# Optimization experiments

Measured on AMD Instinct MI355X. Metric: run time of the kernel, lower is better.

## Reference

```python
import jax, jax.numpy as jnp
import numpy as np

EPS = 1e-5
LOCAL_WINDOW = 256
NUM_HEADS = 16


def _layernorm(x, g, b):
    m = jnp.mean(x, axis=-1, keepdims=True)
    v = jnp.mean(jnp.square(x - m), axis=-1, keepdims=True)
    return (x - m) * jax.lax.rsqrt(v + EPS) * g + b


def _rotate_half(x):
    x1, x2 = jnp.split(x, 2, axis=-1)
    return jnp.concatenate([-x2, x1], axis=-1)


def _rope_cos_sin(s, d, base=10000.0):
    half = d // 2
    inv_freq = 1.0 / base ** (jnp.arange(half, dtype=jnp.float32) / float(half))
    t = jnp.arange(s, dtype=jnp.float32)
    freqs = jnp.einsum('s,d->sd', t, inv_freq)          # [s, half]
    emb = jnp.concatenate([freqs, freqs], axis=-1)       # [s, d]
    return jnp.cos(emb)[None, None, :, :], jnp.sin(emb)[None, None, :, :]


def setup_inputs() -> dict:
    key = jax.random.key(0)
    ks = jax.random.split(key, 8)
    B, S, D, F = 2, 2048, 1024, 4096
    sc = lambda d: 1.0 / np.sqrt(d)
    return {
        'x': jax.random.normal(ks[0], (B, S, D), jnp.float32),
        'w_qkv': jax.random.normal(ks[1], (D, 3 * D), jnp.float32) * sc(D),
        'w_out': jax.random.normal(ks[2], (D, D), jnp.float32) * sc(D),
        'g1': jnp.ones((D,), jnp.float32),
        'b1': jnp.zeros((D,), jnp.float32),
        'g2': jnp.ones((D,), jnp.float32),
        'b2': jnp.zeros((D,), jnp.float32),
        'w_gate': jax.random.normal(ks[3], (D, F), jnp.float32) * sc(D),
        'b_gate': jnp.zeros((F,), jnp.float32),
        'w_up': jax.random.normal(ks[4], (D, F), jnp.float32) * sc(D),
        'b_up': jnp.zeros((F,), jnp.float32),
        'w_down': jax.random.normal(ks[5], (F, D), jnp.float32) * sc(F),
        'b_down': jnp.zeros((D,), jnp.float32),
    }


def reference(x, w_qkv, w_out, g1, b1, g2, b2, w_gate, b_gate, w_up, b_up, w_down, b_down):
    B, S, D = x.shape
    H = NUM_HEADS
    hd = D // H

    # ---- pre-norm + RoPE self-attention ----
    y = _layernorm(x, g1, b1)
    qkv = jnp.einsum('bsd,de->bse', y, w_qkv)
    q, k, v = jnp.split(qkv, 3, axis=-1)
    split_heads = lambda t: t.reshape(B, S, H, hd).transpose(0, 2, 1, 3)  # [b,h,s,hd]
    q, k, v = split_heads(q), split_heads(k), split_heads(v)

    cos, sin = _rope_cos_sin(S, hd)
    q = q * cos + _rotate_half(q) * sin
    k = k * cos + _rotate_half(k) * sin

    scale = float(hd) ** -0.5
    logits = jnp.einsum('bhid,bhjd->bhij', q, k) * scale

    i = jnp.arange(S)[:, None]
    j = jnp.arange(S)[None, :]
    can = (jnp.abs(j - i) <= LOCAL_WINDOW) & (j <= i)    # local + causal band
    logits = jnp.where(can[None, None], logits, jnp.float32(-1e9))

    attn = jax.nn.softmax(logits, axis=-1)
    o = jnp.einsum('bhij,bhjd->bhid', attn, v)
    o = o.transpose(0, 2, 1, 3).reshape(B, S, D)
    x = x + jnp.einsum('bsd,de->bse', o, w_out)

    # ---- pre-norm + SwiGLU MLP ----
    y = _layernorm(x, g2, b2)
    gate = jnp.einsum('bsd,df->bsf', y, w_gate) + b_gate
    up = jnp.einsum('bsd,df->bsf', y, w_up) + b_up
    gated = gate * jax.nn.silu(up)
    x = x + jnp.einsum('bsf,fd->bsd', gated, w_down) + b_down
    return x
```

## Files before the change

kernel.cpp:

```cpp
#include <hip/hip_runtime.h>

typedef unsigned short u16;
typedef unsigned long long u64;
typedef __attribute__((ext_vector_type(8))) short bf16x8;
typedef __attribute__((ext_vector_type(4))) float f32x4;

__device__ inline u16 f2bf(float f) {
  unsigned int u = __float_as_uint(f);
  u += 0x7fffu + ((u >> 16) & 1u);
  return (u16)(u >> 16);
}
__device__ inline float bf2f(u16 h) { return __uint_as_float(((unsigned int)h) << 16); }

__device__ inline void gload_lds16(const void* gp, void* lp) {
  __builtin_amdgcn_global_load_lds(
      (const __attribute__((address_space(1))) unsigned int*)gp,
      (__attribute__((address_space(3))) unsigned int*)lp, 16, 0, 0);
}

__global__ __launch_bounds__(256) void ln_kernel(const float* __restrict__ x,
                                                 const float* __restrict__ g,
                                                 const float* __restrict__ beta,
                                                 u16* __restrict__ y) {
  __shared__ float red[8];
  const int row = blockIdx.x;
  const int t = threadIdx.x;
  const float4 xv = *(const float4*)(x + (long)row * 1024 + t * 4);
  float s = xv.x + xv.y + xv.z + xv.w;
  float sq = xv.x * xv.x + xv.y * xv.y + xv.z * xv.z + xv.w * xv.w;
#pragma unroll
  for (int d = 1; d < 64; d <<= 1) {
    s += __shfl_xor(s, d);
    sq += __shfl_xor(sq, d);
  }
  if ((t & 63) == 0) { red[t >> 6] = s; red[4 + (t >> 6)] = sq; }
  __syncthreads();
  s = red[0] + red[1] + red[2] + red[3];
  sq = red[4] + red[5] + red[6] + red[7];
  const float mean = s * (1.f / 1024.f);
  const float var = sq * (1.f / 1024.f) - mean * mean;
  const float inv = rsqrtf(var + 1e-5f);
  float xe[4] = {xv.x, xv.y, xv.z, xv.w};
  u16 ov[4];
#pragma unroll
  for (int e = 0; e < 4; ++e)
    ov[e] = f2bf((xe[e] - mean) * inv * g[t * 4 + e] + beta[t * 4 + e]);
  *(u64*)(y + (long)row * 1024 + t * 4) = *(u64*)ov;
}

__global__ __launch_bounds__(256) void transpose_bf16(const float* __restrict__ in,
                                                      u16* __restrict__ out,
                                                      int R, int C) {
  __shared__ float tile[64][33];
  const int t = threadIdx.x;
  const int tx = t & 31, ty = t >> 5;
  const int rx = t & 63, cy = t >> 6;
  const long r0 = (long)blockIdx.y * 64, c0 = (long)blockIdx.x * 32;
#pragma unroll
  for (int i = 0; i < 8; ++i)
    tile[ty + i * 8][tx] = in[(r0 + ty + i * 8) * C + c0 + tx];
  __syncthreads();
#pragma unroll
  for (int i = 0; i < 8; ++i)
    out[(c0 + i * 4 + cy) * R + r0 + rx] = f2bf(tile[rx][i * 4 + cy]);
}

__global__ __launch_bounds__(256) void transpose_v(const u16* __restrict__ vv,
                                                   u16* __restrict__ vt) {
  __shared__ u16 tile[64][72];
  const int bh = blockIdx.y;
  const long s0 = (long)blockIdx.x * 64;
  const int t = threadIdx.x;
  const int r = t >> 3, cc = (t & 7) * 8;
  const long src = ((long)(bh >> 4) * 2048 + s0) * 1024 + (bh & 15) * 64;
  *(bf16x8*)&tile[r][cc] = *(const bf16x8*)(vv + src + (long)r * 1024 + cc);
  *(bf16x8*)&tile[r + 32][cc] = *(const bf16x8*)(vv + src + (long)(r + 32) * 1024 + cc);
  __syncthreads();
  const int d = t >> 3, sx = (t & 7) * 8;
  u16 o0[8], o1[8];
#pragma unroll
  for (int e = 0; e < 8; ++e) { o0[e] = tile[sx + e][d]; o1[e] = tile[sx + e][d + 32]; }
  const long dst = (long)bh * 64 * 2048 + s0;
  *(bf16x8*)(vt + dst + (long)d * 2048 + sx) = *(bf16x8*)o0;
  *(bf16x8*)(vt + dst + (long)(d + 32) * 2048 + sx) = *(bf16x8*)o1;
}

__global__ __launch_bounds__(256) void rope_kernel(const u16* __restrict__ qkv,
                                                   u16* __restrict__ qr,
                                                   u16* __restrict__ kr,
                                                   u16* __restrict__ vv) {
  const int row = blockIdx.x;
  const int s = row & 2047;
  const int t = threadIdx.x;
  const u16* base = qkv + (long)row * 3072;
  const long orow = (long)row * 1024;
#pragma unroll
  for (int rep = 0; rep < 2; ++rep) {
    const int p = rep * 256 + t;
    const int h = p >> 5, d0 = p & 31;
    const float inv = exp2f((float)d0 * (-13.287712379549449f / 32.f));
    const float ang = (float)s * inv;
    float sn, cs;
    sincosf(ang, &sn, &cs);
    const int c1 = h * 64 + d0, c2 = c1 + 32;
    float x1 = bf2f(base[c1]), x2 = bf2f(base[c2]);
    qr[orow + c1] = f2bf((x1 * cs - x2 * sn) * 0.125f);
    qr[orow + c2] = f2bf((x2 * cs + x1 * sn) * 0.125f);
    float y1 = bf2f(base[1024 + c1]), y2 = bf2f(base[1024 + c2]);
    kr[orow + c1] = f2bf(y1 * cs - y2 * sn);
    kr[orow + c2] = f2bf(y2 * cs + y1 * sn);
  }
  *(u64*)(vv + orow + t * 4) = *(const u64*)(base + 2048 + t * 4);
}

__global__ __launch_bounds__(64, 4) void attn_kernel(const u16* __restrict__ qr,
                                                     const u16* __restrict__ kr,
                                                     const u16* __restrict__ vt,
                                                     u16* __restrict__ o) {
  __shared__ __attribute__((aligned(16))) u16 Pl[16][40];
  int wg = blockIdx.x;
  wg = (wg & 7) * 512 + (wg >> 3);
  const int qt = wg & 127;
  const int bh = wg >> 7;
  const int qs = qt * 16;
  const int l = threadIdx.x;
  const int lr = l & 15, lg = l >> 4;
  const long bho = (long)(bh >> 4) * 2048 * 1024 + (long)(bh & 15) * 64;
  const long vtb = (long)bh * 64 * 2048;

  const u16* qp = qr + bho + (long)(qs + lr) * 1024 + lg * 8;
  const bf16x8 aq0 = *(const bf16x8*)qp;
  const bf16x8 aq1 = *(const bf16x8*)(qp + 32);

  f32x4 oacc[4];
#pragma unroll
  for (int nt = 0; nt < 4; ++nt) { oacc[nt][0] = 0.f; oacc[nt][1] = 0.f; oacc[nt][2] = 0.f; oacc[nt][3] = 0.f; }
  float m_[4], ls[4];
#pragma unroll
  for (int r = 0; r < 4; ++r) { m_[r] = -1e30f; ls[r] = 0.f; }

  for (int ch = 0; ch < 9; ++ch) {
    const int j0 = qs - 256 + ch * 32;
    if (j0 + 32 <= 0) continue;

    const int jc0u = j0 + lr;
    const int jc1u = j0 + 16 + lr;
    const int jc0 = min(max(jc0u, 0), 2047);
    const int jc1 = min(max(jc1u, 0), 2047);
    const u16* kp0 = kr + bho + (long)jc0 * 1024 + lg * 8;
    const u16* kp1 = kr + bho + (long)jc1 * 1024 + lg * 8;
    const bf16x8 b00 = *(const bf16x8*)kp0;
    const bf16x8 b01 = *(const bf16x8*)(kp0 + 32);
    const bf16x8 b10 = *(const bf16x8*)kp1;
    const bf16x8 b11 = *(const bf16x8*)(kp1 + 32);

    f32x4 z; z[0] = 0.f; z[1] = 0.f; z[2] = 0.f; z[3] = 0.f;
    f32x4 s0 = __builtin_amdgcn_mfma_f32_16x16x32_bf16(aq0, b00, z, 0, 0, 0);
    s0 = __builtin_amdgcn_mfma_f32_16x16x32_bf16(aq1, b01, s0, 0, 0, 0);
    f32x4 s1 = __builtin_amdgcn_mfma_f32_16x16x32_bf16(aq0, b10, z, 0, 0, 0);
    s1 = __builtin_amdgcn_mfma_f32_16x16x32_bf16(aq1, b11, s1, 0, 0, 0);

    float p0[4], p1[4], al[4];
#pragma unroll
    for (int r = 0; r < 4; ++r) {
      const int qg = qs + lg * 4 + r;
      const bool v0 = (jc0u >= 0) & (jc0u <= qg) & (qg - jc0u <= 256);
      const bool v1 = (jc1u >= 0) & (jc1u <= qg) & (qg - jc1u <= 256);
      const float t0 = v0 ? s0[r] : -1e30f;
      const float t1 = v1 ? s1[r] : -1e30f;
      float mx = fmaxf(t0, t1);
      mx = fmaxf(mx, __shfl_xor(mx, 1));
      mx = fmaxf(mx, __shfl_xor(mx, 2));
      mx = fmaxf(mx, __shfl_xor(mx, 4));
      mx = fmaxf(mx, __shfl_xor(mx, 8));
      const float mn = fmaxf(m_[r], mx);
      if (mn < -1e29f) {
        al[r] = 1.f; p0[r] = 0.f; p1[r] = 0.f;
      } else {
        al[r] = __expf(m_[r] - mn);
        p0[r] = (t0 < -1e29f) ? 0.f : __expf(t0 - mn);
        p1[r] = (t1 < -1e29f) ? 0.f : __expf(t1 - mn);
      }
      m_[r] = mn;
      float rs = p0[r] + p1[r];
      rs += __shfl_xor(rs, 1);
      rs += __shfl_xor(rs, 2);
      rs += __shfl_xor(rs, 4);
      rs += __shfl_xor(rs, 8);
      ls[r] = ls[r] * al[r] + rs;
    }
#pragma unroll
    for (int r = 0; r < 4; ++r) {
      Pl[lg * 4 + r][lr] = f2bf(p0[r]);
      Pl[lg * 4 + r][lr + 16] = f2bf(p1[r]);
    }
    asm volatile("s_waitcnt lgkmcnt(0)" ::: "memory");
    const bf16x8 pa = *(const bf16x8*)(&Pl[lr][lg * 8]);

    const int jb = min(max(j0 + lg * 8, 0), 2040);
    const u16* vp = vt + vtb + (long)lr * 2048 + jb;
#pragma unroll
    for (int nt = 0; nt < 4; ++nt) {
      const bf16x8 bv = *(const bf16x8*)(vp + (long)(nt * 16) * 2048);
      f32x4 oa = oacc[nt];
#pragma unroll
      for (int r = 0; r < 4; ++r) oa[r] *= al[r];
      oacc[nt] = __builtin_amdgcn_mfma_f32_16x16x32_bf16(pa, bv, oa, 0, 0, 0);
    }
  }
#pragma unroll
  for (int nt = 0; nt < 4; ++nt)
#pragma unroll
    for (int r = 0; r < 4; ++r) {
      const long qg = qs + lg * 4 + r;
      o[bho + qg * 1024 + nt * 16 + lr] = f2bf(oacc[nt][r] / ls[r]);
    }
}

__device__ __forceinline__ void stage_half(u16* lds, int ldsbase,
                                           const u16* gp, int ld, int col,
                                           int tid, int w) {
  const int r0 = tid >> 3;
  const int sw = ((tid & 7) ^ (r0 & 7)) << 3;
  gload_lds16(gp + (long)r0 * ld + col + sw, lds + ldsbase + w * 512);
  gload_lds16(gp + (long)(r0 + 64) * ld + col + sw, lds + ldsbase + 4096 + w * 512);
}

template <int EPI>
__global__ __launch_bounds__(512, 2) void gemm8p(const u16* __restrict__ A,
                                                 const u16* __restrict__ BT,
                                                 u16* __restrict__ Cb,
                                                 const float* __restrict__ bias,
                                                 const u16* __restrict__ gate,
                                                 int M, int N, int K) {
  __shared__ __attribute__((aligned(16))) u16 lds[65536];
  const int tid = threadIdx.x;
  const int w = tid >> 6, l = tid & 63;
  const int lr = l & 15, lg = l >> 4;
  const int l7 = l & 7;
  const int wr = w >> 2, wc = w & 3;
  const int nbx = N >> 8;
  int wg = blockIdx.x;
  { const int cpx = gridDim.x >> 3; wg = (wg & 7) * cpx + (wg >> 3); }
  const long m0 = (long)(wg / nbx) * 256;
  const long n0 = (long)(wg % nbx) * 256;
  const int NT = K >> 6;

  f32x4 acc[8][4];
#pragma unroll
  for (int i = 0; i < 8; ++i)
#pragma unroll
    for (int j = 0; j < 4; ++j) { acc[i][j][0] = 0.f; acc[i][j][1] = 0.f; acc[i][j][2] = 0.f; acc[i][j][3] = 0.f; }

  const u16* Alo = A + m0 * K;
  const u16* Ahi = A + (m0 + 128) * K;
  const u16* Blo = BT + n0 * K;
  const u16* Bhi = BT + (n0 + 128) * K;

  stage_half(lds, 0, Alo, K, 0, tid, w);
  stage_half(lds, 8192, Ahi, K, 0, tid, w);
  stage_half(lds, 32768, Blo, K, 0, tid, w);
  stage_half(lds, 40960, Bhi, K, 0, tid, w);
  stage_half(lds, 49152, Blo, K, 64, tid, w);
  stage_half(lds, 57344, Bhi, K, 64, tid, w);
  asm volatile("s_waitcnt vmcnt(4)" ::: "memory");
  __builtin_amdgcn_s_barrier();

  for (int t = 0; t < NT; ++t) {
    const int p = t & 1;
    const int baA = (p * 2 + wr) * 8192;
    const int bB = 32768 + p * 16384;
    bf16x8 b[4][2];
#pragma unroll
    for (int q = 0; q < 4; ++q) {
      bf16x8 a[2][2];
#pragma unroll
      for (int m2 = 0; m2 < 2; ++m2) {
        const int rowA = (q * 2 + m2) * 16 + lr;
#pragma unroll
        for (int kh = 0; kh < 2; ++kh)
          a[m2][kh] = *(const bf16x8*)(lds + baA + rowA * 64 + (((kh * 4 + lg) ^ l7) << 3));
      }
      if (q == 0) {
#pragma unroll
        for (int fn = 0; fn < 4; ++fn) {
          const int rb = wc * 64 + fn * 16 + lr;
#pragma unroll
          for (int kh = 0; kh < 2; ++kh)
            b[fn][kh] = *(const bf16x8*)(lds + bB + (rb >> 7) * 8192 + (rb & 127) * 64 + (((kh * 4 + lg) ^ l7) << 3));
        }
      }
      if (q == 0 && t + 1 < NT) stage_half(lds, ((p ^ 1) * 2 + 0) * 8192, Alo, K, (t + 1) * 64, tid, w);
      if (q == 1 && t + 1 < NT) stage_half(lds, ((p ^ 1) * 2 + 1) * 8192, Ahi, K, (t + 1) * 64, tid, w);
      if (q == 2 && t + 2 < NT) stage_half(lds, 32768 + (p * 2 + 0) * 8192, Blo, K, (t + 2) * 64, tid, w);
      if (q == 3 && t + 2 < NT) stage_half(lds, 32768 + (p * 2 + 1) * 8192, Bhi, K, (t + 2) * 64, tid, w);

      __builtin_amdgcn_s_barrier();
      asm volatile("s_waitcnt lgkmcnt(0)" ::: "memory");
      __builtin_amdgcn_s_setprio(1);
#pragma unroll
      for (int m2 = 0; m2 < 2; ++m2)
#pragma unroll
        for (int fn = 0; fn < 4; ++fn)
#pragma unroll
          for (int kh = 0; kh < 2; ++kh)
            acc[q * 2 + m2][fn] = __builtin_amdgcn_mfma_f32_16x16x32_bf16(a[m2][kh], b[fn][kh], acc[q * 2 + m2][fn], 0, 0, 0);
      __builtin_amdgcn_s_setprio(0);
      if (q == 3) {
        if (t + 2 < NT) { asm volatile("s_waitcnt vmcnt(4)" ::: "memory"); }
        else            { asm volatile("s_waitcnt vmcnt(0)" ::: "memory"); }
      }
      __builtin_amdgcn_s_barrier();
    }
  }

#pragma unroll
  for (int fm = 0; fm < 8; ++fm) {
    const long mr = m0 + wr * 128 + fm * 16 + lg * 4;
#pragma unroll
    for (int fn = 0; fn < 4; ++fn) {
      const long nc = n0 + wc * 64 + fn * 16 + lr;
#pragma unroll
      for (int r = 0; r < 4; ++r) {
        const long idx = (mr + r) * N + nc;
        const float v = acc[fm][fn][r];
        if constexpr (EPI == 5) {
          Cb[idx] = f2bf(v);
        } else if constexpr (EPI == 2) {
          Cb[idx] = f2bf(v + bias[nc]);
        } else {
          const float u = v + bias[nc];
          const float sg = 1.f / (1.f + __expf(-u));
          Cb[idx] = f2bf(bf2f(gate[idx]) * u * sg);
        }
      }
    }
  }
}

template <int EPI>
__global__ __launch_bounds__(256) void gemm_bt(const u16* __restrict__ A,
                                               const u16* __restrict__ BT,
                                               float* __restrict__ Cf,
                                               const float* __restrict__ res,
                                               int M, int N, int Kl, int lda, int ldb) {
  __shared__ __attribute__((aligned(16))) u16 As[2][128 * 32];
  __shared__ __attribute__((aligned(16))) u16 Bs[2][128 * 32];
  const int t = threadIdx.x;
  const int w = t >> 6, l = t & 63;
  const int lr = l & 15, lg = l >> 4;
  const int wm = (w >> 1) * 64, wn = (w & 1) * 64;
  const long m0 = (long)blockIdx.y * 128, n0 = (long)blockIdx.x * 128;
  const long koff = (long)blockIdx.z * Kl;
  if constexpr (EPI == 0) Cf += (long)blockIdx.z * M * N;

  f32x4 acc[4][4];
#pragma unroll
  for (int i = 0; i < 4; ++i)
#pragma unroll
    for (int j = 0; j < 4; ++j) { acc[i][j][0] = 0.f; acc[i][j][1] = 0.f; acc[i][j][2] = 0.f; acc[i][j][3] = 0.f; }

  const int row0 = t >> 2, k80 = (t & 3) << 3;
  const int row1 = (256 + t) >> 2, k81 = ((256 + t) & 3) << 3;
  const u16* Ab = A + m0 * lda + koff;
  const u16* Bb = BT + n0 * ldb + koff;

  gload_lds16(Ab + (long)row0 * lda + k80, (u16*)As[0] + w * 512);
  gload_lds16(Ab + (long)row1 * lda + k81, (u16*)As[0] + 2048 + w * 512);
  gload_lds16(Bb + (long)row0 * ldb + k80, (u16*)Bs[0] + w * 512);
  gload_lds16(Bb + (long)row1 * ldb + k81, (u16*)Bs[0] + 2048 + w * 512);
  __syncthreads();

  int cur = 0;
  for (int kt = 0; kt < Kl; kt += 32) {
    if (kt + 32 < Kl) {
      const int nxt = cur ^ 1;
      gload_lds16(Ab + (long)row0 * lda + kt + 32 + k80, (u16*)As[nxt] + w * 512);
      gload_lds16(Ab + (long)row1 * lda + kt + 32 + k81, (u16*)As[nxt] + 2048 + w * 512);
      gload_lds16(Bb + (long)row0 * ldb + kt + 32 + k80, (u16*)Bs[nxt] + w * 512);
      gload_lds16(Bb + (long)row1 * ldb + kt + 32 + k81, (u16*)Bs[nxt] + 2048 + w * 512);
    }
    bf16x8 af[4], bfr[4];
#pragma unroll
    for (int i = 0; i < 4; ++i)
      af[i] = *(const bf16x8*)(As[cur] + (wm + i * 16 + lr) * 32 + lg * 8);
#pragma unroll
    for (int j = 0; j < 4; ++j)
      bfr[j] = *(const bf16x8*)(Bs[cur] + (wn + j * 16 + lr) * 32 + lg * 8);
#pragma unroll
    for (int i = 0; i < 4; ++i)
#pragma unroll
      for (int j = 0; j < 4; ++j)
        acc[i][j] = __builtin_amdgcn_mfma_f32_16x16x32_bf16(af[i], bfr[j], acc[i][j], 0, 0, 0);
    __syncthreads();
    cur ^= 1;
  }

#pragma unroll
  for (int i = 0; i < 4; ++i) {
    const long mr = m0 + wm + i * 16 + lg * 4;
#pragma unroll
    for (int j = 0; j < 4; ++j) {
      const long nc = n0 + wn + j * 16 + lr;
#pragma unroll
      for (int r = 0; r < 4; ++r) {
        const long idx = (mr + r) * N + nc;
        if constexpr (EPI == 0) Cf[idx] = acc[i][j][r];
        else                    Cf[idx] = acc[i][j][r] + res[idx];
      }
    }
  }
}

__global__ __launch_bounds__(256) void combine_kernel(const float* __restrict__ p,
                                                      const float* __restrict__ res,
                                                      const float* __restrict__ bias,
                                                      float* __restrict__ out,
                                                      long total) {
  const long i = ((long)blockIdx.x * 256 + threadIdx.x) * 4;
  if (i >= total) return;
  const float4 a = *(const float4*)(p + i);
  const float4 b = *(const float4*)(p + total + i);
  const float4 r = *(const float4*)(res + i);
  float4 o;
  o.x = a.x + b.x + r.x;
  o.y = a.y + b.y + r.y;
  o.z = a.z + b.z + r.z;
  o.w = a.w + b.w + r.w;
  if (bias) {
    const float4 bb = *(const float4*)(bias + (int)(i & 1023));
    o.x += bb.x; o.y += bb.y; o.z += bb.z; o.w += bb.w;
  }
  *(float4*)(out + i) = o;
}

extern "C" void kernel_launch(void* const* d_in, const int* in_sizes, int n_in,
                              void* d_out, int out_size, void* d_ws, size_t ws_size,
                              hipStream_t stream) {
  (void)in_sizes; (void)n_in; (void)out_size; (void)ws_size;
  const float* x      = (const float*)d_in[0];
  const float* w_qkv  = (const float*)d_in[1];
  const float* w_out  = (const float*)d_in[2];
  const float* g1     = (const float*)d_in[3];
  const float* b1     = (const float*)d_in[4];
  const float* g2     = (const float*)d_in[5];
  const float* b2     = (const float*)d_in[6];
  const float* w_gate = (const float*)d_in[7];
  const float* b_gate = (const float*)d_in[8];
  const float* b_up   = (const float*)d_in[10];
  const float* w_up   = (const float*)d_in[9];
  const float* w_down = (const float*)d_in[11];
  const float* b_down = (const float*)d_in[12];
  float* out = (float*)d_out;

  const size_t MB = 1u << 20;
  char* ws = (char*)d_ws;
  u16*   y      = (u16*)(ws + 0 * MB);
  u16*   wqkvT  = (u16*)(ws + 8 * MB);
  u16*   woutT  = (u16*)(ws + 14 * MB);
  u16*   wgateT = (u16*)(ws + 16 * MB);
  u16*   wupT   = (u16*)(ws + 24 * MB);
  u16*   wdownT = (u16*)(ws + 32 * MB);
  u16*   qkv    = (u16*)(ws + 40 * MB);
  u16*   vt     = (u16*)(ws + 40 * MB);
  float* part   = (float*)(ws + 40 * MB);
  u16*   gbuf   = (u16*)(ws + 40 * MB);
  u16*   qr_    = (u16*)(ws + 88 * MB);
  u16*   kr_    = (u16*)(ws + 96 * MB);
  u16*   vv_    = (u16*)(ws + 104 * MB);
  u16*   o_     = (u16*)(ws + 112 * MB);
  float* x1     = (float*)(ws + 120 * MB);
  u16*   gated  = (u16*)(ws + 88 * MB);

  const dim3 blk(256);
  transpose_bf16<<<dim3(3072 / 32, 1024 / 64), blk, 0, stream>>>(w_qkv, wqkvT, 1024, 3072);
  transpose_bf16<<<dim3(1024 / 32, 1024 / 64), blk, 0, stream>>>(w_out, woutT, 1024, 1024);
  transpose_bf16<<<dim3(4096 / 32, 1024 / 64), blk, 0, stream>>>(w_gate, wgateT, 1024, 4096);
  transpose_bf16<<<dim3(4096 / 32, 1024 / 64), blk, 0, stream>>>(w_up, wupT, 1024, 4096);
  transpose_bf16<<<dim3(1024 / 32, 4096 / 64), blk, 0, stream>>>(w_down, wdownT, 4096, 1024);

  ln_kernel<<<4096, blk, 0, stream>>>(x, g1, b1, y);
  gemm8p<5><<<dim3((3072 / 256) * (4096 / 256)), dim3(512), 0, stream>>>(
      y, wqkvT, qkv, nullptr, nullptr, 4096, 3072, 1024);
  rope_kernel<<<4096, blk, 0, stream>>>(qkv, qr_, kr_, vv_);
  transpose_v<<<dim3(32, 32), blk, 0, stream>>>(vv_, vt);
  attn_kernel<<<4096, dim3(64), 0, stream>>>(qr_, kr_, vt, o_);
  gemm_bt<0><<<dim3(1024 / 128, 4096 / 128, 2), blk, 0, stream>>>(
      o_, woutT, part, nullptr, 4096, 1024, 512, 1024, 1024);
  combine_kernel<<<4096, blk, 0, stream>>>(part, x, nullptr, x1, (long)4096 * 1024);
  ln_kernel<<<4096, blk, 0, stream>>>(x1, g2, b2, y);
  gemm8p<2><<<dim3((4096 / 256) * (4096 / 256)), dim3(512), 0, stream>>>(
      y, wgateT, gbuf, b_gate, nullptr, 4096, 4096, 1024);
  gemm8p<3><<<dim3((4096 / 256) * (4096 / 256)), dim3(512), 0, stream>>>(
      y, wupT, gated, b_up, gbuf, 4096, 4096, 1024);
  gemm_bt<0><<<dim3(1024 / 128, 4096 / 128, 2), blk, 0, stream>>>(
      gated, wdownT, part, nullptr, 4096, 1024, 2048, 4096, 4096);
  combine_kernel<<<4096, blk, 0, stream>>>(part, x1, b_down, out, (long)4096 * 1024);
}
```

Measured before the change: 295.3 us.

## Use pipelined 256x256 GEMM with 4-way split-K for out/down projections, fuse combine+LN

Replaces the simple 128x128 double-buffered split-K GEMM for the attention output and MLP down projections with the heavily pipelined 256x256 gemm8p kernel, extended to split K four ways into fp32 partial buffers. The residual combine and the second layernorm are fused into one kernel, removing a separate pass over x1. It adds a new fp32 write path and a reshuffled workspace layout in which several buffers alias each other, and it doubles the partial-sum traffic compared with 2-way split.

After: 287.3 us. 1.03x faster.

```diff
diff --git a/kernel.cpp b/kernel.cpp
--- a/kernel.cpp
+++ b/kernel.cpp
@@ -232,19 +232,24 @@
                                                  u16* __restrict__ Cb,
                                                  const float* __restrict__ bias,
                                                  const u16* __restrict__ gate,
-                                                 int M, int N, int K) {
+                                                 float* __restrict__ Cf0,
+                                                 float* __restrict__ Cf1,
+                                                 int M, int N, int Kfull, int Kl) {
   __shared__ __attribute__((aligned(16))) u16 lds[65536];
   const int tid = threadIdx.x;
   const int w = tid >> 6, l = tid & 63;
   const int lr = l & 15, lg = l >> 4;
   const int l7 = l & 7;
   const int wr = w >> 2, wc = w & 3;
-  const int nbx = N >> 8;
+  const int nbx = N >> 8, nby = M >> 8;
   int wg = blockIdx.x;
   { const int cpx = gridDim.x >> 3; wg = (wg & 7) * cpx + (wg >> 3); }
-  const long m0 = (long)(wg / nbx) * 256;
-  const long n0 = (long)(wg % nbx) * 256;
-  const int NT = K >> 6;
+  const int z = wg / (nbx * nby);
+  const int rem = wg % (nbx * nby);
+  const long m0 = (long)(rem / nbx) * 256;
+  const long n0 = (long)(rem % nbx) * 256;
+  const long koff = (long)z * Kl;
+  const int NT = Kl >> 6;
 
   f32x4 acc[8][4];
 #pragma unroll
@@ -252,17 +257,17 @@
 #pragma unroll
     for (int j = 0; j < 4; ++j) { acc[i][j][0] = 0.f; acc[i][j][1] = 0.f; acc[i][j][2] = 0.f; acc[i][j][3] = 0.f; }
 
-  const u16* Alo = A + m0 * K;
-  const u16* Ahi = A + (m0 + 128) * K;
-  const u16* Blo = BT + n0 * K;
-  const u16* Bhi = BT + (n0 + 128) * K;
-
-  stage_half(lds, 0, Alo, K, 0, tid, w);
-  stage_half(lds, 8192, Ahi, K, 0, tid, w);
-  stage_half(lds, 32768, Blo, K, 0, tid, w);
-  stage_half(lds, 40960, Bhi, K, 0, tid, w);
-  stage_half(lds, 49152, Blo, K, 64, tid, w);
-  stage_half(lds, 57344, Bhi, K, 64, tid, w);
+  const u16* Alo = A + m0 * Kfull + koff;
+  const u16* Ahi = A + (m0 + 128) * Kfull + koff;
+  const u16* Blo = BT + n0 * Kfull + koff;
+  const u16* Bhi = BT + (n0 + 128) * Kfull + koff;
+
+  stage_half(lds, 0, Alo, Kfull, 0, tid, w);
+  stage_half(lds, 8192, Ahi, Kfull, 0, tid, w);
+  stage_half(lds, 32768, Blo, Kfull, 0, tid, w);
+  stage_half(lds, 40960, Bhi, Kfull, 0, tid, w);
+  stage_half(lds, 49152, Blo, Kfull, 64, tid, w);
+  stage_half(lds, 57344, Bhi, Kfull, 64, tid, w);
   asm volatile("s_waitcnt vmcnt(4)" ::: "memory");
   __builtin_amdgcn_s_barrier();
 
@@ -290,10 +295,10 @@
             b[fn][kh] = *(const bf16x8*)(lds + bB + (rb >> 7) * 8192 + (rb & 127) * 64 + (((kh * 4 + lg) ^ l7) << 3));
         }
       }
-      if (q == 0 && t + 1 < NT) stage_half(lds, ((p ^ 1) * 2 + 0) * 8192, Alo, K, (t + 1) * 64, tid, w);
-      if (q == 1 && t + 1 < NT) stage_half(lds, ((p ^ 1) * 2 + 1) * 8192, Ahi, K, (t + 1) * 64, tid, w);
-      if (q == 2 && t + 2 < NT) stage_half(lds, 32768 + (p * 2 + 0) * 8192, Blo, K, (t + 2) * 64, tid, w);
-      if (q == 3 && t + 2 < NT) stage_half(lds, 32768 + (p * 2 + 1) * 8192, Bhi, K, (t + 2) * 64, tid, w);
+      if (q == 0 && t + 1 < NT) stage_half(lds, ((p ^ 1) * 2 + 0) * 8192, Alo, Kfull, (t + 1) * 64, tid, w);
+      if (q == 1 && t + 1 < NT) stage_half(lds, ((p ^ 1) * 2 + 1) * 8192, Ahi, Kfull, (t + 1) * 64, tid, w);
+      if (q == 2 && t + 2 < NT) stage_half(lds, 32768 + (p * 2 + 0) * 8192, Blo, Kfull, (t + 2) * 64, tid, w);
+      if (q == 3 && t + 2 < NT) stage_half(lds, 32768 + (p * 2 + 1) * 8192, Bhi, Kfull, (t + 2) * 64, tid, w);
 
       __builtin_amdgcn_s_barrier();
       asm volatile("s_waitcnt lgkmcnt(0)" ::: "memory");
@@ -314,6 +319,9 @@
     }
   }
 
+  float* Cf = nullptr;
+  if constexpr (EPI == 0) Cf = (z < 2 ? Cf0 : Cf1) + (long)(z & 1) * M * N;
+
 #pragma unroll
   for (int fm = 0; fm < 8; ++fm) {
     const long mr = m0 + wr * 128 + fm * 16 + lg * 4;
@@ -328,109 +336,77 @@
           Cb[idx] = f2bf(v);
         } else if constexpr (EPI == 2) {
           Cb[idx] = f2bf(v + bias[nc]);
-        } else {
+        } else if constexpr (EPI == 3) {
           const float u = v + bias[nc];
           const float sg = 1.f / (1.f + __expf(-u));
           Cb[idx] = f2bf(bf2f(gate[idx]) * u * sg);
+        } else {
+          Cf[idx] = v;
         }
       }
     }
   }
 }
 
-template <int EPI>
-__global__ __launch_bounds__(256) void gemm_bt(const u16* __restrict__ A,
-                                               const u16* __restrict__ BT,
-                                               float* __restrict__ Cf,
-                                               const float* __restrict__ res,
-                                               int M, int N, int Kl, int lda, int ldb) {
-  __shared__ __attribute__((aligned(16))) u16 As[2][128 * 32];
-  __shared__ __attribute__((aligned(16))) u16 Bs[2][128 * 32];
+__global__ __launch_bounds__(256) void combine_ln(const float* __restrict__ p0,
+                                                  const float* __restrict__ p1,
+                                                  const float* __restrict__ x,
+                                                  const float* __restrict__ g,
+                                                  const float* __restrict__ beta,
+                                                  float* __restrict__ x1,
+                                                  u16* __restrict__ y) {
+  __shared__ float red[8];
+  const long MN = (long)4096 * 1024;
+  const int row = blockIdx.x;
   const int t = threadIdx.x;
-  const int w = t >> 6, l = t & 63;
-  const int lr = l & 15, lg = l >> 4;
-  const int wm = (w >> 1) * 64, wn = (w & 1) * 64;
-  const long m0 = (long)blockIdx.y * 128, n0 = (long)blockIdx.x * 128;
-  const long koff = (long)blockIdx.z * Kl;
-  if constexpr (EPI == 0) Cf += (long)blockIdx.z * M * N;
-
-  f32x4 acc[4][4];
-#pragma unroll
-  for (int i = 0; i < 4; ++i)
-#pragma unroll
-    for (int j = 0; j < 4; ++j) { acc[i][j][0] = 0.f; acc[i][j][1] = 0.f; acc[i][j][2] = 0.f; acc[i][j][3] = 0.f; }
-
-  const int row0 = t >> 2, k80 = (t & 3) << 3;
-  const int row1 = (256 + t) >> 2, k81 = ((256 + t) & 3) << 3;
-  const u16* Ab = A + m0 * lda + koff;
-  const u16* Bb = BT + n0 * ldb + koff;
-
-  gload_lds16(Ab + (long)row0 * lda + k80, (u16*)As[0] + w * 512);
-  gload_lds16(Ab + (long)row1 * lda + k81, (u16*)As[0] + 2048 + w * 512);
-  gload_lds16(Bb + (long)row0 * ldb + k80, (u16*)Bs[0] + w * 512);
-  gload_lds16(Bb + (long)row1 * ldb + k81, (u16*)Bs[0] + 2048 + w * 512);
+  const long base = (long)row * 1024 + t * 4;
+  const float4 a = *(const float4*)(p0 + base);
+  const float4 b = *(const float4*)(p0 + MN + base);
+  const float4 c = *(const float4*)(p1 + base);
+  const float4 d = *(const float4*)(p1 + MN + base);
+  const float4 r = *(const float4*)(x + base);
+  float v[4] = {a.x + b.x + c.x + d.x + r.x, a.y + b.y + c.y + d.y + r.y,
+                a.z + b.z + c.z + d.z + r.z, a.w + b.w + c.w + d.w + r.w};
+  *(float4*)(x1 + base) = *(float4*)v;
+  float s = v[0] + v[1] + v[2] + v[3];
+  float sq = v[0] * v[0] + v[1] * v[1] + v[2] * v[2] + v[3] * v[3];
+#pragma unroll
+  for (int dd = 1; dd < 64; dd <<= 1) {
+    s += __shfl_xor(s, dd);
+    sq += __shfl_xor(sq, dd);
+  }
+  if ((t & 63) == 0) { red[t >> 6] = s; red[4 + (t >> 6)] = sq; }
   __syncthreads();
-
-  int cur = 0;
-  for (int kt = 0; kt < Kl; kt += 32) {
-    if (kt + 32 < Kl) {
-      const int nxt = cur ^ 1;
-      gload_lds16(Ab + (long)row0 * lda + kt + 32 + k80, (u16*)As[nxt] + w * 512);
-      gload_lds16(Ab + (long)row1 * lda + kt + 32 + k81, (u16*)As[nxt] + 2048 + w * 512);
-      gload_lds16(Bb + (long)row0 * ldb + kt + 32 + k80, (u16*)Bs[nxt] + w * 512);
-      gload_lds16(Bb + (long)row1 * ldb + kt + 32 + k81, (u16*)Bs[nxt] + 2048 + w * 512);
-    }
-    bf16x8 af[4], bfr[4];
-#pragma unroll
-    for (int i = 0; i < 4; ++i)
-      af[i] = *(const bf16x8*)(As[cur] + (wm + i * 16 + lr) * 32 + lg * 8);
-#pragma unroll
-    for (int j = 0; j < 4; ++j)
-      bfr[j] = *(const bf16x8*)(Bs[cur] + (wn + j * 16 + lr) * 32 + lg * 8);
-#pragma unroll
-    for (int i = 0; i < 4; ++i)
-#pragma unroll
-      for (int j = 0; j < 4; ++j)
-        acc[i][j] = __builtin_amdgcn_mfma_f32_16x16x32_bf16(af[i], bfr[j], acc[i][j], 0, 0, 0);
-    __syncthreads();
-    cur ^= 1;
-  }
-
-#pragma unroll
-  for (int i = 0; i < 4; ++i) {
-    const long mr = m0 + wm + i * 16 + lg * 4;
-#pragma unroll
-    for (int j = 0; j < 4; ++j) {
-      const long nc = n0 + wn + j * 16 + lr;
-#pragma unroll
-      for (int r = 0; r < 4; ++r) {
-        const long idx = (mr + r) * N + nc;
-        if constexpr (EPI == 0) Cf[idx] = acc[i][j][r];
-        else                    Cf[idx] = acc[i][j][r] + res[idx];
-      }
-    }
-  }
-}
-
-__global__ __launch_bounds__(256) void combine_kernel(const float* __restrict__ p,
-                                                      const float* __restrict__ res,
-                                                      const float* __restrict__ bias,
-                                                      float* __restrict__ out,
-                                                      long total) {
+  s = red[0] + red[1] + red[2] + red[3];
+  sq = red[4] + red[5] + red[6] + red[7];
+  const float mean = s * (1.f / 1024.f);
+  const float var = sq * (1.f / 1024.f) - mean * mean;
+  const float inv = rsqrtf(var + 1e-5f);
+  u16 ov[4];
+#pragma unroll
+  for (int e = 0; e < 4; ++e)
+    ov[e] = f2bf((v[e] - mean) * inv * g[t * 4 + e] + beta[t * 4 + e]);
+  *(u64*)(y + base) = *(u64*)ov;
+}
+
+__global__ __launch_bounds__(256) void combine4(const float* __restrict__ p0,
+                                                const float* __restrict__ p1,
+                                                const float* __restrict__ res,
+                                                const float* __restrict__ bias,
+                                                float* __restrict__ out) {
+  const long MN = (long)4096 * 1024;
   const long i = ((long)blockIdx.x * 256 + threadIdx.x) * 4;
-  if (i >= total) return;
-  const float4 a = *(const float4*)(p + i);
-  const float4 b = *(const float4*)(p + total + i);
+  const float4 a = *(const float4*)(p0 + i);
+  const float4 b = *(const float4*)(p0 + MN + i);
+  const float4 c = *(const float4*)(p1 + i);
+  const float4 d = *(const float4*)(p1 + MN + i);
   const float4 r = *(const float4*)(res + i);
+  const float4 bb = *(const float4*)(bias + (int)(i & 1023));
   float4 o;
-  o.x = a.x + b.x + r.x;
-  o.y = a.y + b.y + r.y;
-  o.z = a.z + b.z + r.z;
-  o.w = a.w + b.w + r.w;
-  if (bias) {
-    const float4 bb = *(const float4*)(bias + (int)(i & 1023));
-    o.x += bb.x; o.y += bb.y; o.z += bb.z; o.w += bb.w;
-  }
+  o.x = a.x + b.x + c.x + d.x + r.x + bb.x;
+  o.y = a.y + b.y + c.y + d.y + r.y + bb.y;
+  o.z = a.z + b.z + c.z + d.z + r.z + bb.z;
+  o.w = a.w + b.w + c.w + d.w + r.w + bb.w;
   *(float4*)(out + i) = o;
 }
 
@@ -447,30 +423,32 @@
   const float* b2     = (const float*)d_in[6];
   const float* w_gate = (const float*)d_in[7];
   const float* b_gate = (const float*)d_in[8];
+  const float* w_up   = (const float*)d_in[9];
   const float* b_up   = (const float*)d_in[10];
-  const float* w_up   = (const float*)d_in[9];
   const float* w_down = (const float*)d_in[11];
   const float* b_down = (const float*)d_in[12];
   float* out = (float*)d_out;
 
   const size_t MB = 1u << 20;
   char* ws = (char*)d_ws;
-  u16*   y      = (u16*)(ws + 0 * MB);
-  u16*   wqkvT  = (u16*)(ws + 8 * MB);
-  u16*   woutT  = (u16*)(ws + 14 * MB);
-  u16*   wgateT = (u16*)(ws + 16 * MB);
-  u16*   wupT   = (u16*)(ws + 24 * MB);
-  u16*   wdownT = (u16*)(ws + 32 * MB);
+  u16*   wdownT = (u16*)(ws + 0 * MB);
+  u16*   y      = (u16*)(ws + 8 * MB);
+  u16*   wqkvT  = (u16*)(ws + 16 * MB);
+  u16*   woutT  = (u16*)(ws + 22 * MB);
+  u16*   wgateT = (u16*)(ws + 24 * MB);
+  u16*   wupT   = (u16*)(ws + 32 * MB);
   u16*   qkv    = (u16*)(ws + 40 * MB);
   u16*   vt     = (u16*)(ws + 40 * MB);
-  float* part   = (float*)(ws + 40 * MB);
-  u16*   gbuf   = (u16*)(ws + 40 * MB);
-  u16*   qr_    = (u16*)(ws + 88 * MB);
-  u16*   kr_    = (u16*)(ws + 96 * MB);
-  u16*   vv_    = (u16*)(ws + 104 * MB);
-  u16*   o_     = (u16*)(ws + 112 * MB);
-  float* x1     = (float*)(ws + 120 * MB);
-  u16*   gated  = (u16*)(ws + 88 * MB);
+  float* x1     = (float*)(ws + 40 * MB);
+  u16*   o_     = (u16*)(ws + 56 * MB);
+  u16*   qr_    = (u16*)(ws + 64 * MB);
+  u16*   kr_    = (u16*)(ws + 72 * MB);
+  u16*   vv_    = (u16*)(ws + 80 * MB);
+  float* part   = (float*)(ws + 64 * MB);
+  u16*   gated  = (u16*)(ws + 64 * MB);
+  u16*   gbuf   = (u16*)(ws + 96 * MB);
+  float* pd0    = (float*)(ws + 8 * MB);
+  float* pd1    = (float*)(ws + 96 * MB);
 
   const dim3 blk(256);
   transpose_bf16<<<dim3(3072 / 32, 1024 / 64), blk, 0, stream>>>(w_qkv, wqkvT, 1024, 3072);
@@ -481,19 +459,19 @@
 
   ln_kernel<<<4096, blk, 0, stream>>>(x, g1, b1, y);
   gemm8p<5><<<dim3((3072 / 256) * (4096 / 256)), dim3(512), 0, stream>>>(
-      y, wqkvT, qkv, nullptr, nullptr, 4096, 3072, 1024);
+      y, wqkvT, qkv, nullptr, nullptr, nullptr, nullptr, 4096, 3072, 1024, 1024);
   rope_kernel<<<4096, blk, 0, stream>>>(qkv, qr_, kr_, vv_);
   transpose_v<<<dim3(32, 32), blk, 0, stream>>>(vv_, vt);
   attn_kernel<<<4096, dim3(64), 0, stream>>>(qr_, kr_, vt, o_);
-  gemm_bt<0><<<dim3(1024 / 128, 4096 / 128, 2), blk, 0, stream>>>(
-      o_, woutT, part, nullptr, 4096, 1024, 512, 1024, 1024);
-  combine_kernel<<<4096, blk, 0, stream>>>(part, x, nullptr, x1, (long)4096 * 1024);
-  ln_kernel<<<4096, blk, 0, stream>>>(x1, g2, b2, y);
+  gemm8p<0><<<dim3(4 * 16 * 4), dim3(512), 0, stream>>>(
+      o_, woutT, nullptr, nullptr, nullptr, part, part + (long)2 * 4096 * 1024,
+      4096, 1024, 1024, 256);
+  combine_ln<<<4096, blk, 0, stream>>>(part, part + (long)2 * 4096 * 1024, x, g2, b2, x1, y);
   gemm8p<2><<<dim3((4096 / 256) * (4096 / 256)), dim3(512), 0, stream>>>(
-      y, wgateT, gbuf, b_gate, nullptr, 4096, 4096, 1024);
+      y, wgateT, gbuf, b_gate, nullptr, nullptr, nullptr, 4096, 4096, 1024, 1024);
   gemm8p<3><<<dim3((4096 / 256) * (4096 / 256)), dim3(512), 0, stream>>>(
-      y, wupT, gated, b_up, gbuf, 4096, 4096, 1024);
-  gemm_bt<0><<<dim3(1024 / 128, 4096 / 128, 2), blk, 0, stream>>>(
-      gated, wdownT, part, nullptr, 4096, 1024, 2048, 4096, 4096);
-  combine_kernel<<<4096, blk, 0, stream>>>(part, x1, b_down, out, (long)4096 * 1024);
-}
+      y, wupT, gated, b_up, gbuf, nullptr, nullptr, 4096, 4096, 1024, 1024);
+  gemm8p<0><<<dim3(4 * 16 * 4), dim3(512), 0, stream>>>(
+      gated, wdownT, nullptr, nullptr, nullptr, pd0, pd1, 4096, 1024, 4096, 1024);
+  combine4<<<4096, blk, 0, stream>>>(pd0, pd1, x1, b_down, out);
+}
```
